# Optimization experiments

Hardware: AMD Instinct MI355X
Metric: run time of the kernel (lower is better)

## Reference

```python
import jax, jax.numpy as jnp
import numpy as np

DIM = 512
HEADS = 8
HEAD_DIM = DIM // HEADS
EPS = 1e-12


def _conv1x1(x, w):
    # x: [B,C,H,W], w: [O,C]
    return jnp.einsum('oc,bchw->bohw', w, x)


def _dwconv3x3(x, w):
    # depthwise 3x3, padding=1. w: [C,1,3,3]
    return jax.lax.conv_general_dilated(
        x, w, window_strides=(1, 1), padding=((1, 1), (1, 1)),
        dimension_numbers=('NCHW', 'OIHW', 'NCHW'),
        feature_group_count=DIM)


def _l2norm(t):
    # normalize along last dim (torch F.normalize semantics)
    n = jnp.sqrt(jnp.sum(t * t, axis=-1, keepdims=True))
    return t / jnp.maximum(n, EPS)


def setup_inputs() -> dict:
    key = jax.random.key(0)
    ks = jax.random.split(key, 6)
    B, C, H, W = 8, DIM, 64, 64
    x = jax.random.normal(ks[0], (B, C, H, W), dtype=jnp.float32)
    # xavier-uniform-ish scale for 1x1 convs: bound = sqrt(6/(C+C))
    b1 = float(np.sqrt(6.0 / (2 * C)))
    q_w = jax.random.uniform(ks[1], (C, C), jnp.float32, -b1, b1)
    k_w = jax.random.uniform(ks[2], (C, C), jnp.float32, -b1, b1)
    v_w = jax.random.uniform(ks[3], (C, C), jnp.float32, -b1, b1)
    proj_w = jax.random.uniform(ks[4], (C, C), jnp.float32, -b1, b1)
    # depthwise 3x3 kernel, default torch conv init scale ~ U(-1/3, 1/3)
    dw_w = jax.random.uniform(ks[5], (C, 1, 3, 3), jnp.float32, -1.0 / 3, 1.0 / 3)
    return {'x': x, 'dw_w': dw_w, 'q_w': q_w, 'k_w': k_w, 'v_w': v_w, 'proj_w': proj_w}


def reference(x, dw_w, q_w, k_w, v_w, proj_w):
    B, C, H, W = x.shape
    scale = HEAD_DIM ** (-0.5)
    x = _dwconv3x3(x, dw_w)
    q = _conv1x1(x, q_w).reshape(B, HEADS, HEAD_DIM, H * W)
    k = _conv1x1(x, k_w).reshape(B, HEADS, HEAD_DIM, H * W)
    v = _conv1x1(x, v_w).reshape(B, HEADS, HEAD_DIM, H * W)
    q = _l2norm(q)
    k = _l2norm(k)
    v = _l2norm(v)
    # transposed (channel) attention: [B,h,hd,hd]
    attn = jnp.einsum('bhdn,bhen->bhde', q, k) * scale
    attn = jax.nn.softmax(attn, axis=-1)
    out = jnp.einsum('bhde,bhen->bhdn', attn, v).reshape(B, C, H, W)
    out = _conv1x1(out, proj_w)
    return out
```

## Files before the change

kernel.cpp:

```cpp
#include <hip/hip_runtime.h>
#include <hip/hip_bf16.h>

#define BATCH 8
#define CDIM 512
#define NPIX 4096
#define NHEAD 8
#define HDIM 64
#define ATT_SCALE 0.125f
#define L2EPS 1e-12f
#define STRIP 8

typedef __attribute__((ext_vector_type(8))) short short8;
typedef __attribute__((ext_vector_type(4))) short bf16x4;
typedef __attribute__((ext_vector_type(4))) float f32x4;

typedef const __attribute__((address_space(1))) void* gas_ptr;
typedef __attribute__((address_space(3))) void* las_ptr;

__device__ __forceinline__ void ld_lds16(const void* g, void* l) {
    __builtin_amdgcn_global_load_lds((gas_ptr)g, (las_ptr)l, 16, 0, 0);
}

__device__ __forceinline__ short f2bs(float f) {
    __hip_bfloat16 h = __float2bfloat16(f);
    return *reinterpret_cast<short*>(&h);
}

__device__ __forceinline__ float bs2f(short s) {
    unsigned u = ((unsigned)(unsigned short)s) << 16;
    return __builtin_bit_cast(float, u);
}

template <int KLEN, int ASTR, int BSTR>
__device__ __forceinline__ void gemm128_core(const short* __restrict__ Ag,
                                             const short* __restrict__ Bg,
                                             short* lds,
                                             f32x4 acc[4][4], int tid) {
    const int wave = tid >> 6, lane = tid & 63;
    const int am = (wave >> 1) * 64, bn = (wave & 1) * 64;
    const int lrow = lane & 15;
    const int kslot = ((lane >> 4) ^ ((lrow >> 1) & 3)) * 8;
    const int sslot = ((lane & 3) ^ ((lane >> 3) & 3)) * 8;
    const int srow = wave * 16 + (lane >> 2);

    {
        short* As = lds;
        short* Bs = lds + 4096;
#pragma unroll
        for (int i = 0; i < 2; ++i) {
            const int r = srow + i * 64;
            const int off = (i * 256 + wave * 64) * 8;
            ld_lds16(Ag + (size_t)r * ASTR + sslot, As + off);
            ld_lds16(Bg + (size_t)r * BSTR + sslot, Bs + off);
        }
    }
    __syncthreads();

    int cur = 0;
    for (int k0 = 0; k0 < KLEN; k0 += 32) {
        if (k0 + 32 < KLEN) {
            short* As = lds + (cur ^ 1) * 8192;
            short* Bs = lds + (cur ^ 1) * 8192 + 4096;
#pragma unroll
            for (int i = 0; i < 2; ++i) {
                const int r = srow + i * 64;
                const int off = (i * 256 + wave * 64) * 8;
                ld_lds16(Ag + (size_t)r * ASTR + (k0 + 32) + sslot, As + off);
                ld_lds16(Bg + (size_t)r * BSTR + (k0 + 32) + sslot, Bs + off);
            }
        }
        const short* As = lds + cur * 8192;
        const short* Bs = lds + cur * 8192 + 4096;
        short8 afrag[4], bfrag[4];
#pragma unroll
        for (int i = 0; i < 4; ++i)
            afrag[i] = *(const short8*)&As[(am + i * 16 + lrow) * 32 + kslot];
#pragma unroll
        for (int j = 0; j < 4; ++j)
            bfrag[j] = *(const short8*)&Bs[(bn + j * 16 + lrow) * 32 + kslot];
#pragma unroll
        for (int i = 0; i < 4; ++i)
#pragma unroll
            for (int j = 0; j < 4; ++j)
                acc[i][j] = __builtin_amdgcn_mfma_f32_16x16x32_bf16(afrag[i], bfrag[j],
                                                                   acc[i][j], 0, 0, 0);
        __syncthreads();
        cur ^= 1;
    }
}

__global__ __launch_bounds__(256) void dwconv_t(const float* __restrict__ x,
                                                const float* __restrict__ w,
                                                short* __restrict__ xd,
                                                short* __restrict__ xdT) {
    __shared__ float tile[16][65];
    const int t = threadIdx.x;
    const int lane = t & 63;
    const int wv = t >> 6;
    const int y0 = blockIdx.x * STRIP;
    const int c0 = blockIdx.y * 16;
    const int b  = blockIdx.z;

    float wgt[4][9];
    float r0[4], r1[4], r2[4];
    const float* xb[4];
#pragma unroll
    for (int i = 0; i < 4; ++i) {
        const int c = c0 + wv * 4 + i;
        const float* wp = w + c * 9;
#pragma unroll
        for (int j = 0; j < 9; ++j) wgt[i][j] = wp[j];
        xb[i] = x + ((size_t)(b * CDIM + c)) * NPIX + lane;
        r0[i] = (y0 > 0) ? xb[i][(y0 - 1) * 64] : 0.f;
        r1[i] = xb[i][y0 * 64];
        r2[i] = xb[i][(y0 + 1) * 64];
    }

    for (int yy = 0; yy < STRIP; ++yy) {
        const int ynext = y0 + yy + 2;
        const bool ldn = (yy < STRIP - 1) && (ynext < 64);
        float nxt[4];
#pragma unroll
        for (int i = 0; i < 4; ++i) nxt[i] = ldn ? xb[i][ynext * 64] : 0.f;

#pragma unroll
        for (int i = 0; i < 4; ++i) {
            float cl = wgt[i][0] * r0[i] + wgt[i][3] * r1[i] + wgt[i][6] * r2[i];
            float cm = wgt[i][1] * r0[i] + wgt[i][4] * r1[i] + wgt[i][7] * r2[i];
            float cr = wgt[i][2] * r0[i] + wgt[i][5] * r1[i] + wgt[i][8] * r2[i];
            float lft = __shfl_up(cl, 1);
            if (lane == 0) lft = 0.f;
            float rgt = __shfl_down(cr, 1);
            if (lane == 63) rgt = 0.f;
            const float val = lft + cm + rgt;
            tile[wv * 4 + i][lane] = val;
            xd[((size_t)(b * CDIM + c0 + wv * 4 + i)) * NPIX + (y0 + yy) * 64 + lane]
                = f2bs(val);
        }
        __syncthreads();
        {
            const int n_l = t >> 2;
            const int cq = (t & 3) * 4;
            bf16x4 pk;
#pragma unroll
            for (int j = 0; j < 4; ++j) pk[j] = f2bs(tile[cq + j][n_l]);
            short* dst = xdT + ((size_t)b * NPIX + (y0 + yy) * 64 + n_l) * CDIM + c0 + cq;
            *(bf16x4*)dst = pk;
        }
        __syncthreads();
#pragma unroll
        for (int i = 0; i < 4; ++i) { r0[i] = r1[i]; r1[i] = r2[i]; r2[i] = nxt[i]; }
    }
}

__global__ __launch_bounds__(256) void cast_weights(const float* __restrict__ s0,
                                                    const float* __restrict__ s1,
                                                    const float* __restrict__ s2,
                                                    const float* __restrict__ s3,
                                                    short* __restrict__ d0,
                                                    short* __restrict__ d1,
                                                    short* __restrict__ d2,
                                                    short* __restrict__ d3,
                                                    short* __restrict__ d4) {
    const int i = blockIdx.x * 256 + threadIdx.x;
    const int m = blockIdx.y;
    if (m < 4) {
        const float* s = (m == 0) ? s0 : (m == 1) ? s1 : (m == 2) ? s2 : s3;
        short* d = (m == 0) ? d0 : (m == 1) ? d1 : (m == 2) ? d2 : d3;
        d[i] = f2bs(s[i]);
    } else {
        d4[i] = f2bs(s2[(size_t)(i & 511) * 512 + (i >> 9)]);
    }
}

__global__ __launch_bounds__(256) void gram_part(const short* __restrict__ xd,
                                                 float* __restrict__ Gp) {
    __shared__ __align__(16) short lds[2 * 8192];
    const int tid = threadIdx.x;
    const int n0 = blockIdx.x * 128;
    const int m0 = blockIdx.y * 128;
    const int z  = blockIdx.z;
    const int b = z >> 2, kh = z & 3;
    const short* Ag = xd + ((size_t)(b * CDIM + m0)) * NPIX + kh * 1024;
    const short* Bg = xd + ((size_t)(b * CDIM + n0)) * NPIX + kh * 1024;
    f32x4 acc[4][4] = {};
    gemm128_core<1024, NPIX, NPIX>(Ag, Bg, lds, acc, tid);

    const int wave = tid >> 6, lane = tid & 63;
    const int am = (wave >> 1) * 64, bn = (wave & 1) * 64;
    const int crow = (lane >> 4) * 4, ccol = lane & 15;
    float* outp = Gp + (size_t)z * 262144;
#pragma unroll
    for (int i = 0; i < 4; ++i)
#pragma unroll
        for (int j = 0; j < 4; ++j)
#pragma unroll
            for (int r = 0; r < 4; ++r)
                outp[(size_t)(m0 + am + i * 16 + crow + r) * 512 + n0 + bn + j * 16 + ccol]
                    = acc[i][j][r];
}

__global__ __launch_bounds__(256) void gram_cast(const float* __restrict__ Gp,
                                                 short* __restrict__ G16) {
    const int i4 = blockIdx.x * 256 + threadIdx.x;
    const int b = i4 >> 16;
    const int r4 = (i4 & 65535) * 4;
    const float* base = Gp + (size_t)(4 * b) * 262144 + r4;
    f32x4 s0 = *(const f32x4*)&base[0];
    f32x4 s1 = *(const f32x4*)&base[262144];
    f32x4 s2 = *(const f32x4*)&base[2 * 262144];
    f32x4 s3 = *(const f32x4*)&base[3 * 262144];
    bf16x4 o;
#pragma unroll
    for (int t = 0; t < 4; ++t) o[t] = f2bs(s0[t] + s1[t] + s2[t] + s3[t]);
    *(bf16x4*)&G16[(size_t)b * 262144 + r4] = o;
}

__global__ __launch_bounds__(256) void gemm_qkvG(const short* __restrict__ Wq,
                                                 const short* __restrict__ Wk,
                                                 const short* __restrict__ Wv,
                                                 const short* __restrict__ G16,
                                                 short* __restrict__ QKVG) {
    __shared__ __align__(16) short lds[2 * 8192];
    const int tid = threadIdx.x;
    const int n0 = blockIdx.x * 128;
    const int ot = blockIdx.y;
    const int g = ot >> 2, o0 = (ot & 3) * 128;
    const int b = blockIdx.z;
    const short* W = (g == 0) ? Wq : (g == 1) ? Wk : Wv;
    const short* Ag = W + (size_t)o0 * CDIM;
    const short* Bg = G16 + (size_t)b * 262144 + (size_t)n0 * 512;
    f32x4 acc[4][4] = {};
    gemm128_core<512, 512, 512>(Ag, Bg, lds, acc, tid);

    const int wave = tid >> 6, lane = tid & 63;
    const int am = (wave >> 1) * 64, bn = (wave & 1) * 64;
    const int crow = (lane >> 4) * 4, ccol = lane & 15;
    short* Yg = QKVG + ((size_t)b * 1536 + g * 512 + o0) * 512;
#pragma unroll
    for (int i = 0; i < 4; ++i)
#pragma unroll
        for (int j = 0; j < 4; ++j)
#pragma unroll
            for (int r = 0; r < 4; ++r)
                Yg[(size_t)(am + i * 16 + crow + r) * 512 + n0 + bn + j * 16 + ccol]
                    = f2bs(acc[i][j][r]);
}

__global__ __launch_bounds__(256) void norms_dot(const short* __restrict__ QKVG,
                                                 const short* __restrict__ Wq,
                                                 const short* __restrict__ Wk,
                                                 const short* __restrict__ Wv,
                                                 float* __restrict__ rnorm) {
    const int tid = threadIdx.x, w = tid >> 6, lane = tid & 63;
#pragma unroll
    for (int it = 0; it < 4; ++it) {
        const int R = blockIdx.x * 16 + w * 4 + it;
        const int b = R / 1536;
        const int mr = R - b * 1536;
        const int m = mr >> 9, row = mr & 511;
        const short* qr = QKVG + (size_t)R * 512 + lane * 8;
        const short* wr = ((m == 0) ? Wq : (m == 1) ? Wk : Wv) + (size_t)row * 512 + lane * 8;
        short8 a = *(const short8*)qr;
        short8 ww = *(const short8*)wr;
        float s = 0.f;
#pragma unroll
        for (int t = 0; t < 8; ++t) s += bs2f(a[t]) * bs2f(ww[t]);
        s += __shfl_xor(s, 1);  s += __shfl_xor(s, 2);
        s += __shfl_xor(s, 4);  s += __shfl_xor(s, 8);
        s += __shfl_xor(s, 16); s += __shfl_xor(s, 32);
        if (lane == 0)
            rnorm[m * 4096 + b * 512 + row] = 1.f / fmaxf(sqrtf(fmaxf(s, 0.f)), L2EPS);
    }
}

__global__ __launch_bounds__(256) void attn_small(const short* __restrict__ QKVG,
                                                  const short* __restrict__ Wk,
                                                  const short* __restrict__ WvT,
                                                  const float* __restrict__ rnorm,
                                                  short* __restrict__ MT) {
    __shared__ __align__(16) short Qs[64 * 32];
    __shared__ __align__(16) short Ks[64 * 32];
    __shared__ __align__(16) short Pl[64 * 72];
    const int tid = threadIdx.x, wave = tid >> 6, lane = tid & 63;
    const int bh = blockIdx.x, b = bh >> 3, h = bh & 7;
    const int lrow = lane & 15;
    const int kslot = ((lane >> 4) ^ ((lrow >> 1) & 3)) * 8;
    const int sslot = ((lane & 3) ^ ((lane >> 3) & 3)) * 8;
    const int srow = tid >> 2;
    const short* qg = QKVG + ((size_t)b * 1536 + h * 64) * 512;
    const short* kg = Wk + (size_t)(h * 64) * 512;
    f32x4 acc[4] = {};
    for (int k0 = 0; k0 < 512; k0 += 32) {
        ld_lds16(qg + (size_t)srow * 512 + k0 + sslot, Qs + wave * 512);
        ld_lds16(kg + (size_t)srow * 512 + k0 + sslot, Ks + wave * 512);
        __syncthreads();
        short8 af = *(const short8*)&Qs[(wave * 16 + lrow) * 32 + kslot];
#pragma unroll
        for (int j = 0; j < 4; ++j) {
            short8 bf = *(const short8*)&Ks[(j * 16 + lrow) * 32 + kslot];
            acc[j] = __builtin_amdgcn_mfma_f32_16x16x32_bf16(af, bf, acc[j], 0, 0, 0);
        }
        __syncthreads();
    }
    const int crow = (lane >> 4) * 4, ccol = lane & 15;
    const float* rq = rnorm + bh * 64;
    const float* rk = rnorm + 4096 + bh * 64;
    const float* rv = rnorm + 8192 + bh * 64;
    float rkv[4], rvv[4];
#pragma unroll
    for (int j = 0; j < 4; ++j) { rkv[j] = rk[j * 16 + ccol]; rvv[j] = rv[j * 16 + ccol]; }
#pragma unroll
    for (int r = 0; r < 4; ++r) {
        const int row = wave * 16 + crow + r;
        const float rqs = ATT_SCALE * rq[row];
        float L[4];
#pragma unroll
        for (int j = 0; j < 4; ++j) L[j] = acc[j][r] * rqs * rkv[j];
        float m = fmaxf(fmaxf(L[0], L[1]), fmaxf(L[2], L[3]));
        m = fmaxf(m, __shfl_xor(m, 1)); m = fmaxf(m, __shfl_xor(m, 2));
        m = fmaxf(m, __shfl_xor(m, 4)); m = fmaxf(m, __shfl_xor(m, 8));
        float p[4], s = 0.f;
#pragma unroll
        for (int j = 0; j < 4; ++j) { p[j] = expf(L[j] - m); s += p[j]; }
        s += __shfl_xor(s, 1); s += __shfl_xor(s, 2);
        s += __shfl_xor(s, 4); s += __shfl_xor(s, 8);
        const float inv = 1.f / s;
#pragma unroll
        for (int j = 0; j < 4; ++j)
            Pl[row * 72 + j * 16 + ccol] = f2bs(p[j] * inv * rvv[j]);
    }
    __syncthreads();
    const int lk2 = (lane >> 4) * 8;
    const short* wvt = WvT + h * 64;
    const int am2 = wave * 128;
    f32x4 acc2[8][4] = {};
#pragma unroll
    for (int ks = 0; ks < 2; ++ks) {
        short8 bfr[4];
#pragma unroll
        for (int j2 = 0; j2 < 4; ++j2)
            bfr[j2] = *(const short8*)&Pl[(j2 * 16 + lrow) * 72 + ks * 32 + lk2];
#pragma unroll
        for (int i2 = 0; i2 < 8; ++i2) {
            short8 afr = *(const short8*)&wvt[(size_t)(am2 + i2 * 16 + lrow) * 512 + ks * 32 + lk2];
#pragma unroll
            for (int j2 = 0; j2 < 4; ++j2)
                acc2[i2][j2] = __builtin_amdgcn_mfma_f32_16x16x32_bf16(afr, bfr[j2],
                                                                      acc2[i2][j2], 0, 0, 0);
        }
    }
#pragma unroll
    for (int i2 = 0; i2 < 8; ++i2)
#pragma unroll
        for (int j2 = 0; j2 < 4; ++j2)
#pragma unroll
            for (int r = 0; r < 4; ++r)
                MT[((size_t)b * 512 + am2 + i2 * 16 + crow + r) * 512 + h * 64 + j2 * 16 + ccol]
                    = f2bs(acc2[i2][j2][r]);
}

__global__ __launch_bounds__(256) void gemm_projF(const short* __restrict__ Wp,
                                                  const short* __restrict__ MT,
                                                  short* __restrict__ F) {
    __shared__ __align__(16) short lds[2 * 8192];
    const int tid = threadIdx.x;
    const int n0 = blockIdx.x * 128;
    const int o0 = blockIdx.y * 128;
    const int b  = blockIdx.z;
    const short* Ag = Wp + (size_t)o0 * CDIM;
    const short* Bg = MT + (size_t)b * 262144 + (size_t)n0 * 512;
    f32x4 acc[4][4] = {};
    gemm128_core<512, 512, 512>(Ag, Bg, lds, acc, tid);

    const int wave = tid >> 6, lane = tid & 63;
    const int am = (wave >> 1) * 64, bn = (wave & 1) * 64;
    const int crow = (lane >> 4) * 4, ccol = lane & 15;
    short* Fg = F + (size_t)b * 262144;
#pragma unroll
    for (int i = 0; i < 4; ++i)
#pragma unroll
        for (int j = 0; j < 4; ++j)
#pragma unroll
            for (int r = 0; r < 4; ++r)
                Fg[(size_t)(o0 + am + i * 16 + crow + r) * 512 + n0 + bn + j * 16 + ccol]
                    = f2bs(acc[i][j][r]);
}

__global__ __launch_bounds__(256) void gemm_final(const short* __restrict__ F,
                                                  const short* __restrict__ XT,
                                                  float* __restrict__ Y) {
    __shared__ __align__(16) short lds[2 * 8192];
    const int tid = threadIdx.x;
    const int n0 = blockIdx.x * 128;
    const int o0 = blockIdx.y * 128;
    const int b  = blockIdx.z;
    const short* Ag = F + (size_t)b * 262144 + (size_t)o0 * 512;
    const short* Bg = XT + ((size_t)b * NPIX + n0) * CDIM;
    f32x4 acc[4][4] = {};
    gemm128_core<512, 512, 512>(Ag, Bg, lds, acc, tid);

    const int wave = tid >> 6, lane = tid & 63;
    const int am = (wave >> 1) * 64, bn = (wave & 1) * 64;
    const int crow = (lane >> 4) * 4, ccol = lane & 15;
#pragma unroll
    for (int i = 0; i < 4; ++i)
#pragma unroll
        for (int j = 0; j < 4; ++j)
#pragma unroll
            for (int r = 0; r < 4; ++r) {
                const int om = o0 + am + i * 16 + crow + r;
                const int on = n0 + bn + j * 16 + ccol;
                Y[((size_t)(b * CDIM + om)) * NPIX + on] = acc[i][j][r];
            }
}

extern "C" void kernel_launch(void* const* d_in, const int* in_sizes, int n_in,
                              void* d_out, int out_size, void* d_ws, size_t ws_size,
                              hipStream_t stream) {
    (void)in_sizes; (void)n_in; (void)out_size; (void)ws_size;
    const float* x      = (const float*)d_in[0];
    const float* dw_w   = (const float*)d_in[1];
    const float* q_w    = (const float*)d_in[2];
    const float* k_w    = (const float*)d_in[3];
    const float* v_w    = (const float*)d_in[4];
    const float* proj_w = (const float*)d_in[5];
    float* out = (float*)d_out;

    const size_t SZ = (size_t)BATCH * CDIM * NPIX;
    short* xd   = (short*)d_ws;
    short* xdT  = xd + SZ;
    float* Gp   = (float*)(xdT + SZ);
    short* G16  = (short*)(Gp + (size_t)32 * 262144);
    short* QKVG = G16 + (size_t)8 * 262144;
    float* rnorm= (float*)(QKVG + (size_t)8 * 1536 * 512);
    short* MTb  = (short*)(rnorm + 12288);
    short* Fb   = MTb + (size_t)8 * 262144;
    short* wqb  = Fb + (size_t)8 * 262144;
    short* wkb  = wqb + 262144;
    short* wvb  = wkb + 262144;
    short* wpb  = wvb + 262144;
    short* wvtb = wpb + 262144;

    dwconv_t<<<dim3(64 / STRIP, CDIM / 16, BATCH), 256, 0, stream>>>(x, dw_w, xd, xdT);

    cast_weights<<<dim3(1024, 5), 256, 0, stream>>>(q_w, k_w, v_w, proj_w,
                                                    wqb, wkb, wvb, wpb, wvtb);

    gram_part<<<dim3(4, 4, 32), 256, 0, stream>>>(xd, Gp);
    gram_cast<<<dim3(2048), 256, 0, stream>>>(Gp, G16);

    gemm_qkvG<<<dim3(4, 12, 8), 256, 0, stream>>>(wqb, wkb, wvb, G16, QKVG);

    norms_dot<<<dim3(768), 256, 0, stream>>>(QKVG, wqb, wkb, wvb, rnorm);

    attn_small<<<dim3(64), 256, 0, stream>>>(QKVG, wkb, wvtb, rnorm, MTb);

    gemm_projF<<<dim3(4, 4, 8), 256, 0, stream>>>(wpb, MTb, Fb);

    gemm_final<<<dim3(32, 4, 8), 256, 0, stream>>>(Fb, xdT, out);
}
```

Measured before the change: 247.9 us.

## Switch GEMMs to 256x256 tiles with 8 waves and triple-buffered LDS pipeline

Replaces the 128x128, 4-wave, double-buffered GEMM core with a 256x256, 8-wave core that keeps three LDS stages in flight using explicit vmcnt waits, split barriers and s_setprio around the MFMA blocks. The gram split-K is widened from 4 to 8 partials and the reduction kernel is updated to match. The aim is more data reuse per tile and better overlap of global-to-LDS loads with MFMA work. In exchange, grids shrink (e.g. 64-256 blocks), which may underfill the 256 CUs, and the larger accumulator array raises register pressure.

```diff
diff --git a/kernel.cpp b/kernel.cpp
--- a/kernel.cpp
+++ b/kernel.cpp
@@ -31,62 +31,77 @@
     return __builtin_bit_cast(float, u);
 }
 
-template <int KLEN, int ASTR, int BSTR>
-__device__ __forceinline__ void gemm128_core(const short* __restrict__ Ag,
+template <int ASTR, int BSTR>
+__device__ __forceinline__ void gemm256_core(const short* __restrict__ Ag,
                                              const short* __restrict__ Bg,
                                              short* lds,
-                                             f32x4 acc[4][4], int tid) {
+                                             f32x4 acc[8][4], int tid) {
     const int wave = tid >> 6, lane = tid & 63;
-    const int am = (wave >> 1) * 64, bn = (wave & 1) * 64;
+    const int wm = wave >> 2, wn = wave & 3;
     const int lrow = lane & 15;
     const int kslot = ((lane >> 4) ^ ((lrow >> 1) & 3)) * 8;
     const int sslot = ((lane & 3) ^ ((lane >> 3) & 3)) * 8;
-    const int srow = wave * 16 + (lane >> 2);
-
-    {
-        short* As = lds;
-        short* Bs = lds + 4096;
-#pragma unroll
-        for (int i = 0; i < 2; ++i) {
-            const int r = srow + i * 64;
-            const int off = (i * 256 + wave * 64) * 8;
-            ld_lds16(Ag + (size_t)r * ASTR + sslot, As + off);
-            ld_lds16(Bg + (size_t)r * BSTR + sslot, Bs + off);
-        }
-    }
-    __syncthreads();
-
-    int cur = 0;
-    for (int k0 = 0; k0 < KLEN; k0 += 32) {
-        if (k0 + 32 < KLEN) {
-            short* As = lds + (cur ^ 1) * 8192;
-            short* Bs = lds + (cur ^ 1) * 8192 + 4096;
-#pragma unroll
-            for (int i = 0; i < 2; ++i) {
-                const int r = srow + i * 64;
-                const int off = (i * 256 + wave * 64) * 8;
-                ld_lds16(Ag + (size_t)r * ASTR + (k0 + 32) + sslot, As + off);
-                ld_lds16(Bg + (size_t)r * BSTR + (k0 + 32) + sslot, Bs + off);
-            }
-        }
-        const short* As = lds + cur * 8192;
-        const short* Bs = lds + cur * 8192 + 4096;
-        short8 afrag[4], bfrag[4];
+    const int srow  = wave * 32 + (lane >> 2);
+    const int NT = 16;
+
+#define STG256(pb, kk) {                                                      \
+        short* A_ = lds + (pb) * 16384;                                       \
+        short* B_ = A_ + 8192;                                                \
+        ld_lds16(Ag + (size_t)srow        * ASTR + (kk) + sslot, A_ + (wave*32     ) * 32); \
+        ld_lds16(Ag + (size_t)(srow + 16) * ASTR + (kk) + sslot, A_ + (wave*32 + 16) * 32); \
+        ld_lds16(Bg + (size_t)srow        * BSTR + (kk) + sslot, B_ + (wave*32     ) * 32); \
+        ld_lds16(Bg + (size_t)(srow + 16) * BSTR + (kk) + sslot, B_ + (wave*32 + 16) * 32); }
+
+    STG256(0, 0)
+    STG256(1, 32)
+    asm volatile("s_waitcnt vmcnt(4)" ::: "memory");
+    __builtin_amdgcn_s_barrier();
+    asm volatile("" ::: "memory");
+
+    for (int t = 0; t < NT; ++t) {
+        const short* A = lds + (t % 3) * 16384;
+        const short* B = A + 8192;
+        if (t + 2 < NT) { STG256((t + 2) % 3, (t + 2) * 32) }
+
+        short8 af[4], bf[4];
 #pragma unroll
         for (int i = 0; i < 4; ++i)
-            afrag[i] = *(const short8*)&As[(am + i * 16 + lrow) * 32 + kslot];
-#pragma unroll
-        for (int j = 0; j < 4; ++j)
-            bfrag[j] = *(const short8*)&Bs[(bn + j * 16 + lrow) * 32 + kslot];
+            af[i] = *(const short8*)&A[(wm * 128 + i * 16 + lrow) * 32 + kslot];
+#pragma unroll
+        for (int j = 0; j < 4; ++j)
+            bf[j] = *(const short8*)&B[(wn * 64 + j * 16 + lrow) * 32 + kslot];
+        asm volatile("" ::: "memory");
+        __builtin_amdgcn_s_barrier();
+        __builtin_amdgcn_s_setprio(1);
 #pragma unroll
         for (int i = 0; i < 4; ++i)
 #pragma unroll
             for (int j = 0; j < 4; ++j)
-                acc[i][j] = __builtin_amdgcn_mfma_f32_16x16x32_bf16(afrag[i], bfrag[j],
+                acc[i][j] = __builtin_amdgcn_mfma_f32_16x16x32_bf16(af[i], bf[j],
                                                                    acc[i][j], 0, 0, 0);
-        __syncthreads();
-        cur ^= 1;
-    }
+        __builtin_amdgcn_s_setprio(0);
+        asm volatile("" ::: "memory");
+        __builtin_amdgcn_s_barrier();
+
+#pragma unroll
+        for (int i = 0; i < 4; ++i)
+            af[i] = *(const short8*)&A[(wm * 128 + (4 + i) * 16 + lrow) * 32 + kslot];
+        asm volatile("" ::: "memory");
+        __builtin_amdgcn_s_barrier();
+        __builtin_amdgcn_s_setprio(1);
+#pragma unroll
+        for (int i = 0; i < 4; ++i)
+#pragma unroll
+            for (int j = 0; j < 4; ++j)
+                acc[4 + i][j] = __builtin_amdgcn_mfma_f32_16x16x32_bf16(af[i], bf[j],
+                                                                       acc[4 + i][j], 0, 0, 0);
+        __builtin_amdgcn_s_setprio(0);
+        if (t + 2 < NT)      { asm volatile("s_waitcnt vmcnt(4)" ::: "memory"); }
+        else if (t + 1 < NT) { asm volatile("s_waitcnt vmcnt(0)" ::: "memory"); }
+        asm volatile("" ::: "memory");
+        __builtin_amdgcn_s_barrier();
+    }
+#undef STG256
 }
 
 __global__ __launch_bounds__(256) void dwconv_t(const float* __restrict__ x,
@@ -173,78 +188,78 @@
     }
 }
 
-__global__ __launch_bounds__(256) void gram_part(const short* __restrict__ xd,
+__global__ __launch_bounds__(512) void gram_part(const short* __restrict__ xd,
                                                  float* __restrict__ Gp) {
-    __shared__ __align__(16) short lds[2 * 8192];
+    __shared__ __align__(16) short lds[3 * 16384];
     const int tid = threadIdx.x;
-    const int n0 = blockIdx.x * 128;
-    const int m0 = blockIdx.y * 128;
+    const int n0 = blockIdx.x * 256;
+    const int m0 = blockIdx.y * 256;
     const int z  = blockIdx.z;
-    const int b = z >> 2, kh = z & 3;
-    const short* Ag = xd + ((size_t)(b * CDIM + m0)) * NPIX + kh * 1024;
-    const short* Bg = xd + ((size_t)(b * CDIM + n0)) * NPIX + kh * 1024;
-    f32x4 acc[4][4] = {};
-    gemm128_core<1024, NPIX, NPIX>(Ag, Bg, lds, acc, tid);
+    const int b = z >> 3, kh = z & 7;
+    const short* Ag = xd + ((size_t)(b * CDIM + m0)) * NPIX + kh * 512;
+    const short* Bg = xd + ((size_t)(b * CDIM + n0)) * NPIX + kh * 512;
+    f32x4 acc[8][4] = {};
+    gemm256_core<NPIX, NPIX>(Ag, Bg, lds, acc, tid);
 
     const int wave = tid >> 6, lane = tid & 63;
-    const int am = (wave >> 1) * 64, bn = (wave & 1) * 64;
+    const int wm = wave >> 2, wn = wave & 3;
     const int crow = (lane >> 4) * 4, ccol = lane & 15;
     float* outp = Gp + (size_t)z * 262144;
 #pragma unroll
-    for (int i = 0; i < 4; ++i)
+    for (int i = 0; i < 8; ++i)
 #pragma unroll
         for (int j = 0; j < 4; ++j)
 #pragma unroll
             for (int r = 0; r < 4; ++r)
-                outp[(size_t)(m0 + am + i * 16 + crow + r) * 512 + n0 + bn + j * 16 + ccol]
-                    = acc[i][j][r];
+                outp[(size_t)(m0 + wm * 128 + i * 16 + crow + r) * 512
+                     + n0 + wn * 64 + j * 16 + ccol] = acc[i][j][r];
 }
 
 __global__ __launch_bounds__(256) void gram_cast(const float* __restrict__ Gp,
                                                  short* __restrict__ G16) {
     const int i4 = blockIdx.x * 256 + threadIdx.x;
     const int b = i4 >> 16;
-    const int r4 = (i4 & 65535) * 4;
-    const float* base = Gp + (size_t)(4 * b) * 262144 + r4;
-    f32x4 s0 = *(const f32x4*)&base[0];
-    f32x4 s1 = *(const f32x4*)&base[262144];
-    f32x4 s2 = *(const f32x4*)&base[2 * 262144];
-    f32x4 s3 = *(const f32x4*)&base[3 * 262144];
+    const int off = (i4 & 65535) * 4;
+    const float* base = Gp + (size_t)(8 * b) * 262144 + off;
+    float s0 = 0.f, s1 = 0.f, s2 = 0.f, s3 = 0.f;
+#pragma unroll
+    for (int kh = 0; kh < 8; ++kh) {
+        f32x4 v = *(const f32x4*)&base[(size_t)kh * 262144];
+        s0 += v[0]; s1 += v[1]; s2 += v[2]; s3 += v[3];
+    }
     bf16x4 o;
-#pragma unroll
-    for (int t = 0; t < 4; ++t) o[t] = f2bs(s0[t] + s1[t] + s2[t] + s3[t]);
-    *(bf16x4*)&G16[(size_t)b * 262144 + r4] = o;
-}
-
-__global__ __launch_bounds__(256) void gemm_qkvG(const short* __restrict__ Wq,
+    o[0] = f2bs(s0); o[1] = f2bs(s1); o[2] = f2bs(s2); o[3] = f2bs(s3);
+    *(bf16x4*)&G16[(size_t)b * 262144 + off] = o;
+}
+
+__global__ __launch_bounds__(512) void gemm_qkvG(const short* __restrict__ Wq,
                                                  const short* __restrict__ Wk,
                                                  const short* __restrict__ Wv,
                                                  const short* __restrict__ G16,
                                                  short* __restrict__ QKVG) {
-    __shared__ __align__(16) short lds[2 * 8192];
+    __shared__ __align__(16) short lds[3 * 16384];
     const int tid = threadIdx.x;
-    const int n0 = blockIdx.x * 128;
-    const int ot = blockIdx.y;
-    const int g = ot >> 2, o0 = (ot & 3) * 128;
-    const int b = blockIdx.z;
-    const short* W = (g == 0) ? Wq : (g == 1) ? Wk : Wv;
-    const short* Ag = W + (size_t)o0 * CDIM;
+    const int n0 = blockIdx.x * 256;
+    const int by = blockIdx.y;
+    const int b  = blockIdx.z;
+    const short* W = (by < 2) ? Wq : (by < 4) ? Wk : Wv;
+    const short* Ag = W + (size_t)(by & 1) * 256 * 512;
     const short* Bg = G16 + (size_t)b * 262144 + (size_t)n0 * 512;
-    f32x4 acc[4][4] = {};
-    gemm128_core<512, 512, 512>(Ag, Bg, lds, acc, tid);
+    f32x4 acc[8][4] = {};
+    gemm256_core<512, 512>(Ag, Bg, lds, acc, tid);
 
     const int wave = tid >> 6, lane = tid & 63;
-    const int am = (wave >> 1) * 64, bn = (wave & 1) * 64;
+    const int wm = wave >> 2, wn = wave & 3;
     const int crow = (lane >> 4) * 4, ccol = lane & 15;
-    short* Yg = QKVG + ((size_t)b * 1536 + g * 512 + o0) * 512;
-#pragma unroll
-    for (int i = 0; i < 4; ++i)
+    short* Yg = QKVG + ((size_t)b * 1536 + by * 256) * 512;
+#pragma unroll
+    for (int i = 0; i < 8; ++i)
 #pragma unroll
         for (int j = 0; j < 4; ++j)
 #pragma unroll
             for (int r = 0; r < 4; ++r)
-                Yg[(size_t)(am + i * 16 + crow + r) * 512 + n0 + bn + j * 16 + ccol]
-                    = f2bs(acc[i][j][r]);
+                Yg[(size_t)(wm * 128 + i * 16 + crow + r) * 512
+                   + n0 + wn * 64 + j * 16 + ccol] = f2bs(acc[i][j][r]);
 }
 
 __global__ __launch_bounds__(256) void norms_dot(const short* __restrict__ QKVG,
@@ -360,57 +375,57 @@
                     = f2bs(acc2[i2][j2][r]);
 }
 
-__global__ __launch_bounds__(256) void gemm_projF(const short* __restrict__ Wp,
+__global__ __launch_bounds__(512) void gemm_projF(const short* __restrict__ Wp,
                                                   const short* __restrict__ MT,
                                                   short* __restrict__ F) {
-    __shared__ __align__(16) short lds[2 * 8192];
+    __shared__ __align__(16) short lds[3 * 16384];
     const int tid = threadIdx.x;
-    const int n0 = blockIdx.x * 128;
-    const int o0 = blockIdx.y * 128;
+    const int n0 = blockIdx.x * 256;
+    const int o0 = blockIdx.y * 256;
     const int b  = blockIdx.z;
     const short* Ag = Wp + (size_t)o0 * CDIM;
     const short* Bg = MT + (size_t)b * 262144 + (size_t)n0 * 512;
-    f32x4 acc[4][4] = {};
-    gemm128_core<512, 512, 512>(Ag, Bg, lds, acc, tid);
+    f32x4 acc[8][4] = {};
+    gemm256_core<512, 512>(Ag, Bg, lds, acc, tid);
 
     const int wave = tid >> 6, lane = tid & 63;
-    const int am = (wave >> 1) * 64, bn = (wave & 1) * 64;
+    const int wm = wave >> 2, wn = wave & 3;
     const int crow = (lane >> 4) * 4, ccol = lane & 15;
     short* Fg = F + (size_t)b * 262144;
 #pragma unroll
-    for (int i = 0; i < 4; ++i)
+    for (int i = 0; i < 8; ++i)
 #pragma unroll
         for (int j = 0; j < 4; ++j)
 #pragma unroll
             for (int r = 0; r < 4; ++r)
-                Fg[(size_t)(o0 + am + i * 16 + crow + r) * 512 + n0 + bn + j * 16 + ccol]
-                    = f2bs(acc[i][j][r]);
-}
-
-__global__ __launch_bounds__(256) void gemm_final(const short* __restrict__ F,
+                Fg[(size_t)(o0 + wm * 128 + i * 16 + crow + r) * 512
+                   + n0 + wn * 64 + j * 16 + ccol] = f2bs(acc[i][j][r]);
+}
+
+__global__ __launch_bounds__(512) void gemm_final(const short* __restrict__ F,
                                                   const short* __restrict__ XT,
                                                   float* __restrict__ Y) {
-    __shared__ __align__(16) short lds[2 * 8192];
+    __shared__ __align__(16) short lds[3 * 16384];
     const int tid = threadIdx.x;
-    const int n0 = blockIdx.x * 128;
-    const int o0 = blockIdx.y * 128;
+    const int n0 = blockIdx.x * 256;
+    const int o0 = blockIdx.y * 256;
     const int b  = blockIdx.z;
     const short* Ag = F + (size_t)b * 262144 + (size_t)o0 * 512;
     const short* Bg = XT + ((size_t)b * NPIX + n0) * CDIM;
-    f32x4 acc[4][4] = {};
-    gemm128_core<512, 512, 512>(Ag, Bg, lds, acc, tid);
+    f32x4 acc[8][4] = {};
+    gemm256_core<512, 512>(Ag, Bg, lds, acc, tid);
 
     const int wave = tid >> 6, lane = tid & 63;
-    const int am = (wave >> 1) * 64, bn = (wave & 1) * 64;
+    const int wm = wave >> 2, wn = wave & 3;
     const int crow = (lane >> 4) * 4, ccol = lane & 15;
 #pragma unroll
-    for (int i = 0; i < 4; ++i)
+    for (int i = 0; i < 8; ++i)
 #pragma unroll
         for (int j = 0; j < 4; ++j)
 #pragma unroll
             for (int r = 0; r < 4; ++r) {
-                const int om = o0 + am + i * 16 + crow + r;
-                const int on = n0 + bn + j * 16 + ccol;
+                const int om = o0 + wm * 128 + i * 16 + crow + r;
+                const int on = n0 + wn * 64 + j * 16 + ccol;
                 Y[((size_t)(b * CDIM + om)) * NPIX + on] = acc[i][j][r];
             }
 }
@@ -431,7 +446,7 @@
     short* xd   = (short*)d_ws;
     short* xdT  = xd + SZ;
     float* Gp   = (float*)(xdT + SZ);
-    short* G16  = (short*)(Gp + (size_t)32 * 262144);
+    short* G16  = (short*)(Gp + (size_t)64 * 262144);
     short* QKVG = G16 + (size_t)8 * 262144;
     float* rnorm= (float*)(QKVG + (size_t)8 * 1536 * 512);
     short* MTb  = (short*)(rnorm + 12288);
@@ -447,16 +462,16 @@
     cast_weights<<<dim3(1024, 5), 256, 0, stream>>>(q_w, k_w, v_w, proj_w,
                                                     wqb, wkb, wvb, wpb, wvtb);
 
-    gram_part<<<dim3(4, 4, 32), 256, 0, stream>>>(xd, Gp);
+    gram_part<<<dim3(2, 2, 64), 512, 0, stream>>>(xd, Gp);
     gram_cast<<<dim3(2048), 256, 0, stream>>>(Gp, G16);
 
-    gemm_qkvG<<<dim3(4, 12, 8), 256, 0, stream>>>(wqb, wkb, wvb, G16, QKVG);
+    gemm_qkvG<<<dim3(2, 6, 8), 512, 0, stream>>>(wqb, wkb, wvb, G16, QKVG);
 
     norms_dot<<<dim3(768), 256, 0, stream>>>(QKVG, wqb, wkb, wvb, rnorm);
 
     attn_small<<<dim3(64), 256, 0, stream>>>(QKVG, wkb, wvtb, rnorm, MTb);
 
-    gemm_projF<<<dim3(4, 4, 8), 256, 0, stream>>>(wpb, MTb, Fb);
-
-    gemm_final<<<dim3(32, 4, 8), 256, 0, stream>>>(Fb, xdT, out);
-}
+    gemm_projF<<<dim3(2, 2, 8), 512, 0, stream>>>(wpb, MTb, Fb);
+
+    gemm_final<<<dim3(16, 2, 8), 512, 0, stream>>>(Fb, xdT, out);
+}
```

New measurement: 262.9 us. 1.06x slower.

## Exploit Gram symmetry to compute only lower-triangular tiles; split attn_small output

Applied to the files above, without the earlier changes.

The Gram matrix X·Xᵀ is symmetric, so gram_part now launches only the 10 lower-triangular 128x128 tile pairs instead of all 16. gram_cast fills the upper triangle by reading the transposed partial sums, using strided loads there. Separately, attn_small is split across 4 blocks in y, each computing a quarter of the WvT·P output rows. This adds parallelism, but every block recomputes the Q·K softmax.

```diff
diff --git a/kernel.cpp b/kernel.cpp
--- a/kernel.cpp
+++ b/kernel.cpp
@@ -177,8 +177,11 @@
                                                  float* __restrict__ Gp) {
     __shared__ __align__(16) short lds[2 * 8192];
     const int tid = threadIdx.x;
-    const int n0 = blockIdx.x * 128;
-    const int m0 = blockIdx.y * 128;
+    int tt = blockIdx.x, ti = 0;
+    while (tt > ti) { tt -= (ti + 1); ++ti; }
+    const int tj = tt;
+    const int m0 = ti * 128;
+    const int n0 = tj * 128;
     const int z  = blockIdx.z;
     const int b = z >> 2, kh = z & 3;
     const short* Ag = xd + ((size_t)(b * CDIM + m0)) * NPIX + kh * 1024;
@@ -204,16 +207,29 @@
                                                  short* __restrict__ G16) {
     const int i4 = blockIdx.x * 256 + threadIdx.x;
     const int b = i4 >> 16;
-    const int r4 = (i4 & 65535) * 4;
-    const float* base = Gp + (size_t)(4 * b) * 262144 + r4;
-    f32x4 s0 = *(const f32x4*)&base[0];
-    f32x4 s1 = *(const f32x4*)&base[262144];
-    f32x4 s2 = *(const f32x4*)&base[2 * 262144];
-    f32x4 s3 = *(const f32x4*)&base[3 * 262144];
+    const int off = (i4 & 65535) * 4;
+    const int r = off >> 9, c4 = off & 511;
+    const float* base = Gp + (size_t)(4 * b) * 262144;
+    float s0 = 0.f, s1 = 0.f, s2 = 0.f, s3 = 0.f;
+    if ((r >> 7) >= (c4 >> 7)) {
+#pragma unroll
+        for (int kh = 0; kh < 4; ++kh) {
+            f32x4 v = *(const f32x4*)&base[(size_t)kh * 262144 + off];
+            s0 += v[0]; s1 += v[1]; s2 += v[2]; s3 += v[3];
+        }
+    } else {
+#pragma unroll
+        for (int kh = 0; kh < 4; ++kh) {
+            const float* p = base + (size_t)kh * 262144 + r;
+            s0 += p[(size_t)(c4 + 0) * 512];
+            s1 += p[(size_t)(c4 + 1) * 512];
+            s2 += p[(size_t)(c4 + 2) * 512];
+            s3 += p[(size_t)(c4 + 3) * 512];
+        }
+    }
     bf16x4 o;
-#pragma unroll
-    for (int t = 0; t < 4; ++t) o[t] = f2bs(s0[t] + s1[t] + s2[t] + s3[t]);
-    *(bf16x4*)&G16[(size_t)b * 262144 + r4] = o;
+    o[0] = f2bs(s0); o[1] = f2bs(s1); o[2] = f2bs(s2); o[3] = f2bs(s3);
+    *(bf16x4*)&G16[(size_t)b * 262144 + off] = o;
 }
 
 __global__ __launch_bounds__(256) void gemm_qkvG(const short* __restrict__ Wq,
@@ -284,6 +300,7 @@
     __shared__ __align__(16) short Pl[64 * 72];
     const int tid = threadIdx.x, wave = tid >> 6, lane = tid & 63;
     const int bh = blockIdx.x, b = bh >> 3, h = bh & 7;
+    const int cq = blockIdx.y;
     const int lrow = lane & 15;
     const int kslot = ((lane >> 4) ^ ((lrow >> 1) & 3)) * 8;
     const int sslot = ((lane & 3) ^ ((lane >> 3) & 3)) * 8;
@@ -333,8 +350,8 @@
     __syncthreads();
     const int lk2 = (lane >> 4) * 8;
     const short* wvt = WvT + h * 64;
-    const int am2 = wave * 128;
-    f32x4 acc2[8][4] = {};
+    const int am2 = cq * 128 + wave * 32;
+    f32x4 acc2[2][4] = {};
 #pragma unroll
     for (int ks = 0; ks < 2; ++ks) {
         short8 bfr[4];
@@ -342,7 +359,7 @@
         for (int j2 = 0; j2 < 4; ++j2)
             bfr[j2] = *(const short8*)&Pl[(j2 * 16 + lrow) * 72 + ks * 32 + lk2];
 #pragma unroll
-        for (int i2 = 0; i2 < 8; ++i2) {
+        for (int i2 = 0; i2 < 2; ++i2) {
             short8 afr = *(const short8*)&wvt[(size_t)(am2 + i2 * 16 + lrow) * 512 + ks * 32 + lk2];
 #pragma unroll
             for (int j2 = 0; j2 < 4; ++j2)
@@ -351,7 +368,7 @@
         }
     }
 #pragma unroll
-    for (int i2 = 0; i2 < 8; ++i2)
+    for (int i2 = 0; i2 < 2; ++i2)
 #pragma unroll
         for (int j2 = 0; j2 < 4; ++j2)
 #pragma unroll
@@ -447,14 +464,14 @@
     cast_weights<<<dim3(1024, 5), 256, 0, stream>>>(q_w, k_w, v_w, proj_w,
                                                     wqb, wkb, wvb, wpb, wvtb);
 
-    gram_part<<<dim3(4, 4, 32), 256, 0, stream>>>(xd, Gp);
+    gram_part<<<dim3(10, 1, 32), 256, 0, stream>>>(xd, Gp);
     gram_cast<<<dim3(2048), 256, 0, stream>>>(Gp, G16);
 
     gemm_qkvG<<<dim3(4, 12, 8), 256, 0, stream>>>(wqb, wkb, wvb, G16, QKVG);
 
     norms_dot<<<dim3(768), 256, 0, stream>>>(QKVG, wqb, wkb, wvb, rnorm);
 
-    attn_small<<<dim3(64), 256, 0, stream>>>(QKVG, wkb, wvtb, rnorm, MTb);
+    attn_small<<<dim3(64, 4), 256, 0, stream>>>(QKVG, wkb, wvtb, rnorm, MTb);
 
     gemm_projF<<<dim3(4, 4, 8), 256, 0, stream>>>(wpb, MTb, Fb);
 
```

New measurement: 266.6 us. +7.5%, slower.

## Process two rows per dwconv iteration and split attn_small output across blocks

Applied to the files above, without the earlier changes.

The depthwise conv kernel now computes two output rows per loop iteration using a double-buffered LDS tile, which halves the number of barrier pairs and issues two row loads together. attn_small is launched with 4x more blocks: each block recomputes the QK^T softmax but handles only a quarter of the WvT×P output rows, so 64 blocks become 256. This trades redundant small GEMM/softmax work for better GPU occupancy and fewer registers per thread.

```diff
diff --git a/kernel.cpp b/kernel.cpp
--- a/kernel.cpp
+++ b/kernel.cpp
@@ -93,7 +93,7 @@
                                                 const float* __restrict__ w,
                                                 short* __restrict__ xd,
                                                 short* __restrict__ xdT) {
-    __shared__ float tile[16][65];
+    __shared__ float tile[2][16][65];
     const int t = threadIdx.x;
     const int lane = t & 63;
     const int wv = t >> 6;
@@ -116,40 +116,62 @@
         r2[i] = xb[i][(y0 + 1) * 64];
     }
 
-    for (int yy = 0; yy < STRIP; ++yy) {
-        const int ynext = y0 + yy + 2;
-        const bool ldn = (yy < STRIP - 1) && (ynext < 64);
-        float nxt[4];
-#pragma unroll
-        for (int i = 0; i < 4; ++i) nxt[i] = ldn ? xb[i][ynext * 64] : 0.f;
-
+    for (int yy = 0; yy < STRIP; yy += 2) {
+        const int y = y0 + yy;
+        const bool l2 = (y + 2 < 64);
+        const bool l3 = (yy < STRIP - 2) && (y + 3 < 64);
+        float nA[4], nB[4];
 #pragma unroll
         for (int i = 0; i < 4; ++i) {
-            float cl = wgt[i][0] * r0[i] + wgt[i][3] * r1[i] + wgt[i][6] * r2[i];
-            float cm = wgt[i][1] * r0[i] + wgt[i][4] * r1[i] + wgt[i][7] * r2[i];
-            float cr = wgt[i][2] * r0[i] + wgt[i][5] * r1[i] + wgt[i][8] * r2[i];
-            float lft = __shfl_up(cl, 1);
-            if (lane == 0) lft = 0.f;
-            float rgt = __shfl_down(cr, 1);
-            if (lane == 63) rgt = 0.f;
-            const float val = lft + cm + rgt;
-            tile[wv * 4 + i][lane] = val;
-            xd[((size_t)(b * CDIM + c0 + wv * 4 + i)) * NPIX + (y0 + yy) * 64 + lane]
-                = f2bs(val);
+            nA[i] = l2 ? xb[i][(y + 2) * 64] : 0.f;
+            nB[i] = l3 ? xb[i][(y + 3) * 64] : 0.f;
+        }
+
+#pragma unroll
+        for (int i = 0; i < 4; ++i) {
+            {
+                float cl = wgt[i][0] * r0[i] + wgt[i][3] * r1[i] + wgt[i][6] * r2[i];
+                float cm = wgt[i][1] * r0[i] + wgt[i][4] * r1[i] + wgt[i][7] * r2[i];
+                float cr = wgt[i][2] * r0[i] + wgt[i][5] * r1[i] + wgt[i][8] * r2[i];
+                float lft = __shfl_up(cl, 1);
+                if (lane == 0) lft = 0.f;
+                float rgt = __shfl_down(cr, 1);
+                if (lane == 63) rgt = 0.f;
+                const float val = lft + cm + rgt;
+                tile[0][wv * 4 + i][lane] = val;
+                xd[((size_t)(b * CDIM + c0 + wv * 4 + i)) * NPIX + y * 64 + lane]
+                    = f2bs(val);
+            }
+            {
+                float cl = wgt[i][0] * r1[i] + wgt[i][3] * r2[i] + wgt[i][6] * nA[i];
+                float cm = wgt[i][1] * r1[i] + wgt[i][4] * r2[i] + wgt[i][7] * nA[i];
+                float cr = wgt[i][2] * r1[i] + wgt[i][5] * r2[i] + wgt[i][8] * nA[i];
+                float lft = __shfl_up(cl, 1);
+                if (lane == 0) lft = 0.f;
+                float rgt = __shfl_down(cr, 1);
+                if (lane == 63) rgt = 0.f;
+                const float val = lft + cm + rgt;
+                tile[1][wv * 4 + i][lane] = val;
+                xd[((size_t)(b * CDIM + c0 + wv * 4 + i)) * NPIX + (y + 1) * 64 + lane]
+                    = f2bs(val);
+            }
         }
         __syncthreads();
         {
             const int n_l = t >> 2;
             const int cq = (t & 3) * 4;
-            bf16x4 pk;
-#pragma unroll
-            for (int j = 0; j < 4; ++j) pk[j] = f2bs(tile[cq + j][n_l]);
-            short* dst = xdT + ((size_t)b * NPIX + (y0 + yy) * 64 + n_l) * CDIM + c0 + cq;
-            *(bf16x4*)dst = pk;
+#pragma unroll
+            for (int s = 0; s < 2; ++s) {
+                bf16x4 pk;
+#pragma unroll
+                for (int j = 0; j < 4; ++j) pk[j] = f2bs(tile[s][cq + j][n_l]);
+                short* dst = xdT + ((size_t)b * NPIX + (y + s) * 64 + n_l) * CDIM + c0 + cq;
+                *(bf16x4*)dst = pk;
+            }
         }
         __syncthreads();
 #pragma unroll
-        for (int i = 0; i < 4; ++i) { r0[i] = r1[i]; r1[i] = r2[i]; r2[i] = nxt[i]; }
+        for (int i = 0; i < 4; ++i) { r0[i] = r2[i]; r1[i] = nA[i]; r2[i] = nB[i]; }
     }
 }
 
@@ -284,6 +306,7 @@
     __shared__ __align__(16) short Pl[64 * 72];
     const int tid = threadIdx.x, wave = tid >> 6, lane = tid & 63;
     const int bh = blockIdx.x, b = bh >> 3, h = bh & 7;
+    const int cq = blockIdx.y;
     const int lrow = lane & 15;
     const int kslot = ((lane >> 4) ^ ((lrow >> 1) & 3)) * 8;
     const int sslot = ((lane & 3) ^ ((lane >> 3) & 3)) * 8;
@@ -333,8 +356,8 @@
     __syncthreads();
     const int lk2 = (lane >> 4) * 8;
     const short* wvt = WvT + h * 64;
-    const int am2 = wave * 128;
-    f32x4 acc2[8][4] = {};
+    const int am2 = cq * 128 + wave * 32;
+    f32x4 acc2[2][4] = {};
 #pragma unroll
     for (int ks = 0; ks < 2; ++ks) {
         short8 bfr[4];
@@ -342,7 +365,7 @@
         for (int j2 = 0; j2 < 4; ++j2)
             bfr[j2] = *(const short8*)&Pl[(j2 * 16 + lrow) * 72 + ks * 32 + lk2];
 #pragma unroll
-        for (int i2 = 0; i2 < 8; ++i2) {
+        for (int i2 = 0; i2 < 2; ++i2) {
             short8 afr = *(const short8*)&wvt[(size_t)(am2 + i2 * 16 + lrow) * 512 + ks * 32 + lk2];
 #pragma unroll
             for (int j2 = 0; j2 < 4; ++j2)
@@ -351,7 +374,7 @@
         }
     }
 #pragma unroll
-    for (int i2 = 0; i2 < 8; ++i2)
+    for (int i2 = 0; i2 < 2; ++i2)
 #pragma unroll
         for (int j2 = 0; j2 < 4; ++j2)
 #pragma unroll
@@ -454,7 +477,7 @@
 
     norms_dot<<<dim3(768), 256, 0, stream>>>(QKVG, wqb, wkb, wvb, rnorm);
 
-    attn_small<<<dim3(64), 256, 0, stream>>>(QKVG, wkb, wvtb, rnorm, MTb);
+    attn_small<<<dim3(64, 4), 256, 0, stream>>>(QKVG, wkb, wvtb, rnorm, MTb);
 
     gemm_projF<<<dim3(4, 4, 8), 256, 0, stream>>>(wpb, MTb, Fb);
 
```

Result: faster. 242.9 us (median of 2 runs) (-2.0%).
